# Kernel tuning notes

Hardware: AMD Instinct MI355X
Metric: run time of the kernel (lower is better)

## Reference

```python
import jax, jax.numpy as jnp
import numpy as np

N = 8192
F_IN = 512
F_HID = 256
ALPHA = 0.2  # LeakyReLU negative slope
NEG_INF = -9e15


def gat_layer(h, adj, W, a):
    """Standard dense GraphAttentionLayer (pyGAT style).
    h: [N, F_in], adj: [N, N] (0/1), W: [F_in, F_out], a: [2*F_out, 1].
    """
    Wh = h @ W  # [N, F_out]
    f_out = W.shape[1]
    # e_ij = leakyrelu(a1 . Wh_i + a2 . Wh_j) via broadcasting
    e1 = Wh @ a[:f_out]      # [N, 1]
    e2 = Wh @ a[f_out:]      # [N, 1]
    e = jax.nn.leaky_relu(e1 + e2.T, negative_slope=ALPHA)  # [N, N]
    e = jnp.where(adj > 0, e, NEG_INF)
    att = jax.nn.softmax(e, axis=-1)  # masked row softmax
    return jax.nn.elu(att @ Wh)       # [N, F_out]


def setup_inputs() -> dict:
    key = jax.random.key(0)
    k_x, k_adj, k_w1, k_a1, k_w2, k_a2 = jax.random.split(key, 6)
    x = jax.random.normal(k_x, (N, F_IN), dtype=jnp.float32)
    # sparse random adjacency (~avg degree 16) + self loops
    adj = (jax.random.uniform(k_adj, (N, N)) < (16.0 / N)).astype(jnp.float32)
    adj = jnp.clip(adj + jnp.eye(N, dtype=jnp.float32), 0.0, 1.0)
    # Xavier-ish init for layer params
    W1 = jax.random.normal(k_w1, (F_IN, F_HID), dtype=jnp.float32) * (1.0 / np.sqrt(F_IN))
    a1 = jax.random.normal(k_a1, (2 * F_HID, 1), dtype=jnp.float32) * (1.0 / np.sqrt(2 * F_HID))
    W2 = jax.random.normal(k_w2, (F_HID, F_IN), dtype=jnp.float32) * (1.0 / np.sqrt(F_HID))
    a2 = jax.random.normal(k_a2, (2 * F_IN, 1), dtype=jnp.float32) * (1.0 / np.sqrt(2 * F_IN))
    return {"x": x, "adj": adj, "W1": W1, "a1": a1, "W2": W2, "a2": a2}


def reference(x, adj, W1, a1, W2, a2):
    enc = gat_layer(x, adj, W1, a1)    # encode: [N, F_HID]
    dec = gat_layer(enc, adj, W2, a2)  # decode: [N, F_IN]
    return (dec, enc)
```

## Files before the change

kernel.cpp:

```cpp
#include <hip/hip_runtime.h>
#include <hip/hip_bf16.h>

#define N_NODES 8192
#define F_IN    512
#define F_HID   256
#define ALPHA   0.2f
#define MAXDEG  64

using f32x4 = __attribute__((ext_vector_type(4))) float;
using f16x8 = __attribute__((ext_vector_type(8))) _Float16;
using f16x4 = __attribute__((ext_vector_type(4))) _Float16;

__global__ void prep_kernel(const float* __restrict__ W1, const float* __restrict__ W2,
                            _Float16* __restrict__ W1T, _Float16* __restrict__ W2T,
                            const float* __restrict__ a2,
                            float* __restrict__ w2s, float* __restrict__ w2t,
                            float* __restrict__ stz) {
    const int tid = threadIdx.x;
    int gid = blockIdx.x * 256 + tid;
    if (gid < 2 * N_NODES) stz[gid] = 0.0f;

    if (blockIdx.x >= 256) {
        const int r = (blockIdx.x - 256) * 64 + (tid >> 2);
        const int q = tid & 3;
        float ss = 0.f, tt = 0.f;
        for (int n = q * 4; n < F_IN; n += 16) {
            f32x4 w  = *(const f32x4*)&W2[(size_t)r * F_IN + n];
            f32x4 as = *(const f32x4*)&a2[n];
            f32x4 at = *(const f32x4*)&a2[F_IN + n];
            #pragma unroll
            for (int j = 0; j < 4; ++j) { ss += w[j] * as[j]; tt += w[j] * at[j]; }
        }
        ss += __shfl_xor(ss, 1); ss += __shfl_xor(ss, 2);
        tt += __shfl_xor(tt, 1); tt += __shfl_xor(tt, 2);
        if (q == 0) { w2s[r] = ss; w2t[r] = tt; }
        return;
    }

    int t = blockIdx.x;
    const float* W; _Float16* WT; int K, N, kt, nt;
    if (t < 128) { W = W1; WT = W1T; K = 512; N = 256; kt = t & 15; nt = t >> 4; }
    else { t -= 128; W = W2; WT = W2T; K = 256; N = 512; kt = t & 7; nt = t >> 3; }
    __shared__ float Ws[32][33];
    const int tx = tid & 31, ty = tid >> 5;
    #pragma unroll
    for (int i = 0; i < 4; ++i)
        Ws[ty + 8 * i][tx] = W[(size_t)(kt * 32 + ty + 8 * i) * N + nt * 32 + tx];
    __syncthreads();
    #pragma unroll
    for (int i = 0; i < 4; ++i)
        WT[(size_t)(nt * 32 + ty + 8 * i) * K + kt * 32 + tx] = (_Float16)Ws[tx][ty + 8 * i];
}

__device__ inline void csr_row(const float* __restrict__ adj, int* __restrict__ cols,
                               int* __restrict__ cnt, int row, int lane) {
    const f32x4* arow = (const f32x4*)(adj + (size_t)row * N_NODES);
    int* crow = cols + (size_t)row * MAXDEG;
    int count = 0;
    const unsigned long long mlt = (1ULL << lane) - 1ULL;
    for (int base = 0; base < N_NODES; base += 512) {
        f32x4 v0 = __builtin_nontemporal_load(&arow[(base >> 2) + lane]);
        f32x4 v1 = __builtin_nontemporal_load(&arow[(base >> 2) + 64 + lane]);
        unsigned long long b0 = __ballot(v0[0] > 0.0f);
        unsigned long long b1 = __ballot(v0[1] > 0.0f);
        unsigned long long b2 = __ballot(v0[2] > 0.0f);
        unsigned long long b3 = __ballot(v0[3] > 0.0f);
        unsigned long long b4 = __ballot(v1[0] > 0.0f);
        unsigned long long b5 = __ballot(v1[1] > 0.0f);
        unsigned long long b6 = __ballot(v1[2] > 0.0f);
        unsigned long long b7 = __ballot(v1[3] > 0.0f);
        int o = count + __popcll(b0 & mlt) + __popcll(b1 & mlt)
                      + __popcll(b2 & mlt) + __popcll(b3 & mlt);
        int c0 = base + (lane << 2);
        if (v0[0] > 0.0f) { if (o < MAXDEG) crow[o] = c0;     o++; }
        if (v0[1] > 0.0f) { if (o < MAXDEG) crow[o] = c0 + 1; o++; }
        if (v0[2] > 0.0f) { if (o < MAXDEG) crow[o] = c0 + 2; o++; }
        if (v0[3] > 0.0f) { if (o < MAXDEG) crow[o] = c0 + 3; o++; }
        count += __popcll(b0) + __popcll(b1) + __popcll(b2) + __popcll(b3);
        o = count + __popcll(b4 & mlt) + __popcll(b5 & mlt)
                  + __popcll(b6 & mlt) + __popcll(b7 & mlt);
        int c1 = base + 256 + (lane << 2);
        if (v1[0] > 0.0f) { if (o < MAXDEG) crow[o] = c1;     o++; }
        if (v1[1] > 0.0f) { if (o < MAXDEG) crow[o] = c1 + 1; o++; }
        if (v1[2] > 0.0f) { if (o < MAXDEG) crow[o] = c1 + 2; o++; }
        if (v1[3] > 0.0f) { if (o < MAXDEG) crow[o] = c1 + 3; o++; }
        count += __popcll(b4) + __popcll(b5) + __popcll(b6) + __popcll(b7);
    }
    if (lane == 0) cnt[row] = count > MAXDEG ? MAXDEG : count;
}

__device__ inline void gemm1_tile(const float* __restrict__ x,
                                  const _Float16* __restrict__ W1T,
                                  _Float16* __restrict__ Wh1,
                                  const float* __restrict__ a1,
                                  float* __restrict__ s1, float* __restrict__ t1,
                                  int brow, int bcol) {
    const int LDT = 72;
    __shared__ _Float16 As[64 * LDT];
    __shared__ _Float16 Bs[128 * LDT];
    const int tid = threadIdx.x;
    const int wid = tid >> 6, lane = tid & 63;
    const int wr = (wid >> 1) * 32, wc = (wid & 1) * 64;
    const int sr = tid >> 3, skg = (tid & 7) * 8;

    f32x4 acc[2][4];
    #pragma unroll
    for (int m = 0; m < 2; ++m)
        #pragma unroll
        for (int n = 0; n < 4; ++n) acc[m][n] = f32x4{0.f, 0.f, 0.f, 0.f};

    for (int k0 = 0; k0 < F_IN; k0 += 64) {
        #pragma unroll
        for (int i = 0; i < 2; ++i) {
            int r = sr + i * 32;
            const f32x4* src = (const f32x4*)(x + (size_t)(brow + r) * F_IN + k0 + skg);
            f32x4 a0 = src[0];
            f32x4 a1v = src[1];
            f16x8 av;
            #pragma unroll
            for (int j = 0; j < 4; ++j) { av[j] = (_Float16)a0[j]; av[4 + j] = (_Float16)a1v[j]; }
            *(f16x8*)&As[r * LDT + skg] = av;
        }
        #pragma unroll
        for (int i = 0; i < 4; ++i) {
            int r = sr + i * 32;
            *(f16x8*)&Bs[r * LDT + skg] =
                *(const f16x8*)&W1T[(size_t)(bcol + r) * F_IN + k0 + skg];
        }
        __syncthreads();
        #pragma unroll
        for (int ks = 0; ks < 2; ++ks) {
            const int kb = ks * 32 + (lane >> 4) * 8;
            f16x8 af[2], bfr[4];
            #pragma unroll
            for (int m = 0; m < 2; ++m)
                af[m] = *(const f16x8*)&As[(wr + m * 16 + (lane & 15)) * LDT + kb];
            #pragma unroll
            for (int n = 0; n < 4; ++n)
                bfr[n] = *(const f16x8*)&Bs[(wc + n * 16 + (lane & 15)) * LDT + kb];
            #pragma unroll
            for (int m = 0; m < 2; ++m)
                #pragma unroll
                for (int n = 0; n < 4; ++n)
                    acc[m][n] = __builtin_amdgcn_mfma_f32_16x16x32_f16(
                        af[m], bfr[n], acc[m][n], 0, 0, 0);
        }
        __syncthreads();
    }
    const int cl = lane & 15;
    float as[4], at[4];
    #pragma unroll
    for (int n = 0; n < 4; ++n) {
        as[n] = a1[bcol + wc + n * 16 + cl];
        at[n] = a1[F_HID + bcol + wc + n * 16 + cl];
    }
    #pragma unroll
    for (int m = 0; m < 2; ++m) {
        #pragma unroll
        for (int j = 0; j < 4; ++j) {
            float vs = 0.f, vt = 0.f;
            #pragma unroll
            for (int n = 0; n < 4; ++n) { vs += acc[m][n][j] * as[n]; vt += acc[m][n][j] * at[n]; }
            #pragma unroll
            for (int off = 1; off < 16; off <<= 1) {
                vs += __shfl_xor(vs, off);
                vt += __shfl_xor(vt, off);
            }
            if (cl == 0) {
                int row = brow + wr + m * 16 + ((lane >> 4) << 2) + j;
                atomicAdd(s1 + row, vs);
                atomicAdd(t1 + row, vt);
            }
        }
        #pragma unroll
        for (int n = 0; n < 4; ++n) {
            int row = brow + wr + m * 16 + ((lane >> 4) << 2);
            int col = bcol + wc + n * 16 + cl;
            #pragma unroll
            for (int j = 0; j < 4; ++j)
                Wh1[(size_t)(row + j) * F_HID + col] = (_Float16)acc[m][n][j];
        }
    }
}

__global__ __launch_bounds__(256)
void csr_and_gemm1(const float* __restrict__ adj, int* __restrict__ cols,
                   int* __restrict__ cnt, const float* __restrict__ x,
                   const _Float16* __restrict__ W1T, _Float16* __restrict__ Wh1,
                   const float* __restrict__ a1,
                   float* __restrict__ s1, float* __restrict__ t1) {
    const int bid = blockIdx.x;
    if (bid < 256) {
        gemm1_tile(x, W1T, Wh1, a1, s1, t1, (bid & 127) * 64, (bid >> 7) * 128);
    } else {
        const int q = bid - 256;
        const int row = q * 4 + (threadIdx.x >> 6);
        csr_row(adj, cols, cnt, row, threadIdx.x & 63);
    }
}

__global__ void aggregate_l1(const _Float16* __restrict__ Wh,
                             const int* __restrict__ cols, const int* __restrict__ cnt,
                             const float* __restrict__ s, const float* __restrict__ t,
                             const float* __restrict__ w2s, const float* __restrict__ w2t,
                             float* __restrict__ enc, _Float16* __restrict__ enc16,
                             float* __restrict__ s2, float* __restrict__ t2) {
    const int wid = threadIdx.x >> 6, lane = threadIdx.x & 63;
    const int row = blockIdx.x * 4 + wid;
    const int deg = cnt[row];
    __shared__ float pS[4][64];
    __shared__ int jS[4][64];
    int j = 0;
    float ev = -1e30f;
    if (lane < deg) {
        j = cols[(size_t)row * MAXDEG + lane];
        float z = s[row] + t[j];
        ev = z > 0.0f ? z : ALPHA * z;
    }
    float m = ev;
    #pragma unroll
    for (int off = 32; off > 0; off >>= 1) m = fmaxf(m, __shfl_xor(m, off));
    float ex = (lane < deg) ? __expf(ev - m) : 0.0f;
    float sum = ex;
    #pragma unroll
    for (int off = 32; off > 0; off >>= 1) sum += __shfl_xor(sum, off);
    pS[wid][lane] = ex / sum;
    jS[wid][lane] = j;
    __syncthreads();

    float acc[4] = {};
    const size_t lo = (size_t)lane * 4;
    int d = 0;
    for (; d + 4 <= deg; d += 4) {
        float p0 = pS[wid][d],     p1 = pS[wid][d + 1];
        float p2 = pS[wid][d + 2], p3 = pS[wid][d + 3];
        f16x4 v0 = *(const f16x4*)(Wh + (size_t)jS[wid][d] * F_HID + lo);
        f16x4 v1 = *(const f16x4*)(Wh + (size_t)jS[wid][d + 1] * F_HID + lo);
        f16x4 v2 = *(const f16x4*)(Wh + (size_t)jS[wid][d + 2] * F_HID + lo);
        f16x4 v3 = *(const f16x4*)(Wh + (size_t)jS[wid][d + 3] * F_HID + lo);
        #pragma unroll
        for (int jj = 0; jj < 4; ++jj)
            acc[jj] += p0 * (float)v0[jj] + p1 * (float)v1[jj]
                     + p2 * (float)v2[jj] + p3 * (float)v3[jj];
    }
    for (; d < deg; ++d) {
        float p = pS[wid][d];
        f16x4 w = *(const f16x4*)(Wh + (size_t)jS[wid][d] * F_HID + lo);
        #pragma unroll
        for (int jj = 0; jj < 4; ++jj) acc[jj] += p * (float)w[jj];
    }
    f32x4 o; f16x4 h;
    #pragma unroll
    for (int jj = 0; jj < 4; ++jj) {
        float v = acc[jj];
        float e = v > 0.0f ? v : (__expf(v) - 1.0f);
        o[jj] = e; h[jj] = (_Float16)e;
    }
    __builtin_nontemporal_store(o, (f32x4*)(enc + (size_t)row * F_HID + lo));
    *(f16x4*)(enc16 + (size_t)row * F_HID + lo) = h;

    f32x4 ws = *(const f32x4*)(w2s + lo);
    f32x4 wt = *(const f32x4*)(w2t + lo);
    float ps = 0.f, pt = 0.f;
    #pragma unroll
    for (int jj = 0; jj < 4; ++jj) { ps += o[jj] * ws[jj]; pt += o[jj] * wt[jj]; }
    #pragma unroll
    for (int off = 32; off > 0; off >>= 1) {
        ps += __shfl_xor(ps, off);
        pt += __shfl_xor(pt, off);
    }
    if (lane == 0) { s2[row] = ps; t2[row] = pt; }
}

__global__ void aggregate_l2pre(const _Float16* __restrict__ enc16,
                                const int* __restrict__ cols, const int* __restrict__ cnt,
                                const float* __restrict__ s, const float* __restrict__ t,
                                _Float16* __restrict__ aggE16) {
    const int wid = threadIdx.x >> 6, lane = threadIdx.x & 63;
    const int row = blockIdx.x * 4 + wid;
    const int deg = cnt[row];
    __shared__ float pS[4][64];
    __shared__ int jS[4][64];
    int j = 0;
    float ev = -1e30f;
    if (lane < deg) {
        j = cols[(size_t)row * MAXDEG + lane];
        float z = s[row] + t[j];
        ev = z > 0.0f ? z : ALPHA * z;
    }
    float m = ev;
    #pragma unroll
    for (int off = 32; off > 0; off >>= 1) m = fmaxf(m, __shfl_xor(m, off));
    float ex = (lane < deg) ? __expf(ev - m) : 0.0f;
    float sum = ex;
    #pragma unroll
    for (int off = 32; off > 0; off >>= 1) sum += __shfl_xor(sum, off);
    pS[wid][lane] = ex / sum;
    jS[wid][lane] = j;
    __syncthreads();

    float acc[4] = {};
    const size_t lo = (size_t)lane * 4;
    int d = 0;
    for (; d + 4 <= deg; d += 4) {
        float p0 = pS[wid][d],     p1 = pS[wid][d + 1];
        float p2 = pS[wid][d + 2], p3 = pS[wid][d + 3];
        f16x4 v0 = *(const f16x4*)(enc16 + (size_t)jS[wid][d] * F_HID + lo);
        f16x4 v1 = *(const f16x4*)(enc16 + (size_t)jS[wid][d + 1] * F_HID + lo);
        f16x4 v2 = *(const f16x4*)(enc16 + (size_t)jS[wid][d + 2] * F_HID + lo);
        f16x4 v3 = *(const f16x4*)(enc16 + (size_t)jS[wid][d + 3] * F_HID + lo);
        #pragma unroll
        for (int jj = 0; jj < 4; ++jj)
            acc[jj] += p0 * (float)v0[jj] + p1 * (float)v1[jj]
                     + p2 * (float)v2[jj] + p3 * (float)v3[jj];
    }
    for (; d < deg; ++d) {
        float p = pS[wid][d];
        f16x4 w = *(const f16x4*)(enc16 + (size_t)jS[wid][d] * F_HID + lo);
        #pragma unroll
        for (int jj = 0; jj < 4; ++jj) acc[jj] += p * (float)w[jj];
    }
    f16x4 h;
    #pragma unroll
    for (int jj = 0; jj < 4; ++jj) h[jj] = (_Float16)acc[jj];
    *(f16x4*)(aggE16 + (size_t)row * F_HID + lo) = h;
}

__global__ __launch_bounds__(256)
void gemm2e(const _Float16* __restrict__ A, const _Float16* __restrict__ BT,
            float* __restrict__ C) {
    const int LDT = 72, LDB = 264;
    __shared__ _Float16 As[128 * LDT];
    __shared__ _Float16 Bs[64 * LDB];
    const int tid = threadIdx.x;
    const int wid = tid >> 6, lane = tid & 63;
    const int brow = (blockIdx.x >> 3) * 128;
    const int bcol = (blockIdx.x & 7) * 64;
    const int wr = (wid >> 1) * 64, wc = (wid & 1) * 32;

    #pragma unroll
    for (int i = 0; i < 8; ++i) {
        int id = tid + i * 256;
        int r = id >> 5, kc = (id & 31) * 8;
        *(f16x8*)&Bs[r * LDB + kc] = *(const f16x8*)&BT[(size_t)(bcol + r) * F_HID + kc];
    }

    f32x4 acc[4][2];
    #pragma unroll
    for (int m = 0; m < 4; ++m)
        #pragma unroll
        for (int n = 0; n < 2; ++n) acc[m][n] = f32x4{0.f, 0.f, 0.f, 0.f};

    for (int k0 = 0; k0 < F_HID; k0 += 64) {
        #pragma unroll
        for (int i = 0; i < 4; ++i) {
            int id = tid + i * 256;
            int r = id >> 3, kc = (id & 7) * 8;
            *(f16x8*)&As[r * LDT + kc] = *(const f16x8*)&A[(size_t)(brow + r) * F_HID + k0 + kc];
        }
        __syncthreads();
        #pragma unroll
        for (int ks = 0; ks < 2; ++ks) {
            const int kb = ks * 32 + (lane >> 4) * 8;
            f16x8 af[4], bfr[2];
            #pragma unroll
            for (int m = 0; m < 4; ++m)
                af[m] = *(const f16x8*)&As[(wr + m * 16 + (lane & 15)) * LDT + kb];
            #pragma unroll
            for (int n = 0; n < 2; ++n)
                bfr[n] = *(const f16x8*)&Bs[(wc + n * 16 + (lane & 15)) * LDB + k0 + kb];
            #pragma unroll
            for (int m = 0; m < 4; ++m)
                #pragma unroll
                for (int n = 0; n < 2; ++n)
                    acc[m][n] = __builtin_amdgcn_mfma_f32_16x16x32_f16(
                        af[m], bfr[n], acc[m][n], 0, 0, 0);
        }
        __syncthreads();
    }
    #pragma unroll
    for (int m = 0; m < 4; ++m)
        #pragma unroll
        for (int n = 0; n < 2; ++n) {
            int row = brow + wr + m * 16 + ((lane >> 4) << 2);
            int col = bcol + wc + n * 16 + (lane & 15);
            #pragma unroll
            for (int j = 0; j < 4; ++j) {
                float v = acc[m][n][j];
                float e = v > 0.0f ? v : (__expf(v) - 1.0f);
                __builtin_nontemporal_store(e, &C[(size_t)(row + j) * F_IN + col]);
            }
        }
}

extern "C" void kernel_launch(void* const* d_in, const int* in_sizes, int n_in,
                              void* d_out, int out_size, void* d_ws, size_t ws_size,
                              hipStream_t stream) {
    (void)in_sizes; (void)n_in; (void)out_size; (void)ws_size;
    const float* x   = (const float*)d_in[0];
    const float* adj = (const float*)d_in[1];
    const float* W1  = (const float*)d_in[2];
    const float* a1  = (const float*)d_in[3];
    const float* W2  = (const float*)d_in[4];
    const float* a2  = (const float*)d_in[5];

    float* dec = (float*)d_out;
    float* enc = dec + (size_t)N_NODES * F_IN;

    int*      cols   = (int*)d_ws;
    int*      cnt    = cols + (size_t)N_NODES * MAXDEG;
    float*    s1     = (float*)(cnt + N_NODES);
    float*    t1     = s1 + N_NODES;
    float*    s2     = t1 + N_NODES;
    float*    t2     = s2 + N_NODES;
    float*    w2s    = t2 + N_NODES;
    float*    w2t    = w2s + F_HID;
    _Float16* Wh1    = (_Float16*)(w2t + F_HID);
    _Float16* enc16  = Wh1 + (size_t)N_NODES * F_HID;
    _Float16* aggE16 = enc16 + (size_t)N_NODES * F_HID;
    _Float16* W1T    = aggE16 + (size_t)N_NODES * F_HID;
    _Float16* W2T    = W1T + (size_t)F_HID * F_IN;

    prep_kernel<<<260, 256, 0, stream>>>(W1, W2, W1T, W2T, a2, w2s, w2t, s1);

    csr_and_gemm1<<<2304, 256, 0, stream>>>(adj, cols, cnt, x, W1T, Wh1, a1, s1, t1);

    aggregate_l1<<<N_NODES / 4, 256, 0, stream>>>(Wh1, cols, cnt, s1, t1,
                                                  w2s, w2t, enc, enc16, s2, t2);

    aggregate_l2pre<<<N_NODES / 4, 256, 0, stream>>>(enc16, cols, cnt, s2, t2, aggE16);

    gemm2e<<<512, 256, 0, stream>>>(aggE16, W2T, dec);
}
```

Before: 100.3 us.

## Fold weight prep into front kernel and replace atomics with partial sums

Removes the separate prep kernel. W1 is now read as fp32 and transposed/converted into shared memory inside the GEMM1 tile, and the W2 transpose and the W2·a2 vectors are computed by extra blocks of the fused front kernel. The atomicAdd accumulation of s1/t1 becomes plain stores into four per-column-partition buffers, which aggregate_l1 sums, so the zero-init pass is no longer needed. This saves one launch and the atomic traffic. In exchange, the in-GEMM transpose does scalar strided shared-memory stores that may bank-conflict, and W1 conversion is repeated by every tile.

```diff
diff --git a/kernel.cpp b/kernel.cpp
--- a/kernel.cpp
+++ b/kernel.cpp
@@ -10,47 +10,6 @@
 using f32x4 = __attribute__((ext_vector_type(4))) float;
 using f16x8 = __attribute__((ext_vector_type(8))) _Float16;
 using f16x4 = __attribute__((ext_vector_type(4))) _Float16;
-
-__global__ void prep_kernel(const float* __restrict__ W1, const float* __restrict__ W2,
-                            _Float16* __restrict__ W1T, _Float16* __restrict__ W2T,
-                            const float* __restrict__ a2,
-                            float* __restrict__ w2s, float* __restrict__ w2t,
-                            float* __restrict__ stz) {
-    const int tid = threadIdx.x;
-    int gid = blockIdx.x * 256 + tid;
-    if (gid < 2 * N_NODES) stz[gid] = 0.0f;
-
-    if (blockIdx.x >= 256) {
-        const int r = (blockIdx.x - 256) * 64 + (tid >> 2);
-        const int q = tid & 3;
-        float ss = 0.f, tt = 0.f;
-        for (int n = q * 4; n < F_IN; n += 16) {
-            f32x4 w  = *(const f32x4*)&W2[(size_t)r * F_IN + n];
-            f32x4 as = *(const f32x4*)&a2[n];
-            f32x4 at = *(const f32x4*)&a2[F_IN + n];
-            #pragma unroll
-            for (int j = 0; j < 4; ++j) { ss += w[j] * as[j]; tt += w[j] * at[j]; }
-        }
-        ss += __shfl_xor(ss, 1); ss += __shfl_xor(ss, 2);
-        tt += __shfl_xor(tt, 1); tt += __shfl_xor(tt, 2);
-        if (q == 0) { w2s[r] = ss; w2t[r] = tt; }
-        return;
-    }
-
-    int t = blockIdx.x;
-    const float* W; _Float16* WT; int K, N, kt, nt;
-    if (t < 128) { W = W1; WT = W1T; K = 512; N = 256; kt = t & 15; nt = t >> 4; }
-    else { t -= 128; W = W2; WT = W2T; K = 256; N = 512; kt = t & 7; nt = t >> 3; }
-    __shared__ float Ws[32][33];
-    const int tx = tid & 31, ty = tid >> 5;
-    #pragma unroll
-    for (int i = 0; i < 4; ++i)
-        Ws[ty + 8 * i][tx] = W[(size_t)(kt * 32 + ty + 8 * i) * N + nt * 32 + tx];
-    __syncthreads();
-    #pragma unroll
-    for (int i = 0; i < 4; ++i)
-        WT[(size_t)(nt * 32 + ty + 8 * i) * K + kt * 32 + tx] = (_Float16)Ws[tx][ty + 8 * i];
-}
 
 __device__ inline void csr_row(const float* __restrict__ adj, int* __restrict__ cols,
                                int* __restrict__ cnt, int row, int lane) {
@@ -90,10 +49,10 @@
 }
 
 __device__ inline void gemm1_tile(const float* __restrict__ x,
-                                  const _Float16* __restrict__ W1T,
+                                  const float* __restrict__ W1,
                                   _Float16* __restrict__ Wh1,
                                   const float* __restrict__ a1,
-                                  float* __restrict__ s1, float* __restrict__ t1,
+                                  float* __restrict__ s1p, float* __restrict__ t1p,
                                   int brow, int bcol) {
     const int LDT = 72;
     __shared__ _Float16 As[64 * LDT];
@@ -121,11 +80,17 @@
             for (int j = 0; j < 4; ++j) { av[j] = (_Float16)a0[j]; av[4 + j] = (_Float16)a1v[j]; }
             *(f16x8*)&As[r * LDT + skg] = av;
         }
-        #pragma unroll
-        for (int i = 0; i < 4; ++i) {
-            int r = sr + i * 32;
-            *(f16x8*)&Bs[r * LDT + skg] =
-                *(const f16x8*)&W1T[(size_t)(bcol + r) * F_IN + k0 + skg];
+        {
+            const int cq = (tid & 31) * 4;
+            const int kbase = tid >> 5;
+            #pragma unroll
+            for (int rd = 0; rd < 8; ++rd) {
+                int krow = kbase + 8 * rd;
+                f32x4 w = *(const f32x4*)&W1[(size_t)(k0 + krow) * F_HID + bcol + cq];
+                #pragma unroll
+                for (int q = 0; q < 4; ++q)
+                    Bs[(cq + q) * LDT + krow] = (_Float16)w[q];
+            }
         }
         __syncthreads();
         #pragma unroll
@@ -148,6 +113,7 @@
         __syncthreads();
     }
     const int cl = lane & 15;
+    const int part = (bcol >> 7) * 2 + (wc >> 6);
     float as[4], at[4];
     #pragma unroll
     for (int n = 0; n < 4; ++n) {
@@ -168,8 +134,8 @@
             }
             if (cl == 0) {
                 int row = brow + wr + m * 16 + ((lane >> 4) << 2) + j;
-                atomicAdd(s1 + row, vs);
-                atomicAdd(t1 + row, vt);
+                s1p[part * N_NODES + row] = vs;
+                t1p[part * N_NODES + row] = vt;
             }
         }
         #pragma unroll
@@ -183,28 +149,144 @@
     }
 }
 
+__device__ inline void w2T_tile(int t, const float* __restrict__ W2,
+                                _Float16* __restrict__ W2T) {
+    __shared__ float Ws[32][33];
+    const int kt = t & 7, nt = t >> 3;
+    const int tx = threadIdx.x & 31, ty = threadIdx.x >> 5;
+    #pragma unroll
+    for (int i = 0; i < 4; ++i)
+        Ws[ty + 8 * i][tx] = W2[(size_t)(kt * 32 + ty + 8 * i) * F_IN + nt * 32 + tx];
+    __syncthreads();
+    #pragma unroll
+    for (int i = 0; i < 4; ++i)
+        W2T[(size_t)(nt * 32 + ty + 8 * i) * F_HID + kt * 32 + tx] = (_Float16)Ws[tx][ty + 8 * i];
+}
+
+__device__ inline void w2vec_job(int t, const float* __restrict__ W2,
+                                 const float* __restrict__ a2,
+                                 float* __restrict__ w2s, float* __restrict__ w2t) {
+    const int r = t * 64 + (threadIdx.x >> 2);
+    const int q = threadIdx.x & 3;
+    float ss = 0.f, tt = 0.f;
+    for (int n = q * 4; n < F_IN; n += 16) {
+        f32x4 w  = *(const f32x4*)&W2[(size_t)r * F_IN + n];
+        f32x4 as = *(const f32x4*)&a2[n];
+        f32x4 at = *(const f32x4*)&a2[F_IN + n];
+        #pragma unroll
+        for (int j = 0; j < 4; ++j) { ss += w[j] * as[j]; tt += w[j] * at[j]; }
+    }
+    ss += __shfl_xor(ss, 1); ss += __shfl_xor(ss, 2);
+    tt += __shfl_xor(tt, 1); tt += __shfl_xor(tt, 2);
+    if (q == 0) { w2s[r] = ss; w2t[r] = tt; }
+}
+
 __global__ __launch_bounds__(256)
-void csr_and_gemm1(const float* __restrict__ adj, int* __restrict__ cols,
-                   int* __restrict__ cnt, const float* __restrict__ x,
-                   const _Float16* __restrict__ W1T, _Float16* __restrict__ Wh1,
-                   const float* __restrict__ a1,
-                   float* __restrict__ s1, float* __restrict__ t1) {
+void front_kernel(const float* __restrict__ adj, int* __restrict__ cols,
+                  int* __restrict__ cnt, const float* __restrict__ x,
+                  const float* __restrict__ W1, const float* __restrict__ a1,
+                  _Float16* __restrict__ Wh1,
+                  float* __restrict__ s1p, float* __restrict__ t1p,
+                  const float* __restrict__ W2, const float* __restrict__ a2,
+                  _Float16* __restrict__ W2T,
+                  float* __restrict__ w2s, float* __restrict__ w2t) {
     const int bid = blockIdx.x;
     if (bid < 256) {
-        gemm1_tile(x, W1T, Wh1, a1, s1, t1, (bid & 127) * 64, (bid >> 7) * 128);
+        gemm1_tile(x, W1, Wh1, a1, s1p, t1p, (bid & 127) * 64, (bid >> 7) * 128);
+    } else if (bid < 384) {
+        w2T_tile(bid - 256, W2, W2T);
+    } else if (bid < 388) {
+        w2vec_job(bid - 384, W2, a2, w2s, w2t);
     } else {
-        const int q = bid - 256;
+        const int q = bid - 388;
         const int row = q * 4 + (threadIdx.x >> 6);
         csr_row(adj, cols, cnt, row, threadIdx.x & 63);
     }
 }
 
-__global__ void aggregate_l1(const _Float16* __restrict__ Wh,
-                             const int* __restrict__ cols, const int* __restrict__ cnt,
-                             const float* __restrict__ s, const float* __restrict__ t,
-                             const float* __restrict__ w2s, const float* __restrict__ w2t,
-                             float* __restrict__ enc, _Float16* __restrict__ enc16,
-                             float* __restrict__ s2, float* __restrict__ t2) {
+__global__ __launch_bounds__(256)
+void aggregate_l1(const _Float16* __restrict__ Wh,
+                  const int* __restrict__ cols, const int* __restrict__ cnt,
+                  const float* __restrict__ s1p, const float* __restrict__ t1p,
+                  const float* __restrict__ w2s, const float* __restrict__ w2t,
+                  float* __restrict__ enc, _Float16* __restrict__ enc16,
+                  float* __restrict__ s2, float* __restrict__ t2) {
+    const int wid = threadIdx.x >> 6, lane = threadIdx.x & 63;
+    const int row = blockIdx.x * 4 + wid;
+    const int deg = cnt[row];
+    __shared__ float pS[4][64];
+    __shared__ int jS[4][64];
+    const float sI = s1p[row] + s1p[N_NODES + row]
+                   + s1p[2 * N_NODES + row] + s1p[3 * N_NODES + row];
+    int j = 0;
+    float ev = -1e30f;
+    if (lane < deg) {
+        j = cols[(size_t)row * MAXDEG + lane];
+        float tj = t1p[j] + t1p[N_NODES + j]
+                 + t1p[2 * N_NODES + j] + t1p[3 * N_NODES + j];
+        float z = sI + tj;
+        ev = z > 0.0f ? z : ALPHA * z;
+    }
+    float m = ev;
+    #pragma unroll
+    for (int off = 32; off > 0; off >>= 1) m = fmaxf(m, __shfl_xor(m, off));
+    float ex = (lane < deg) ? __expf(ev - m) : 0.0f;
+    float sum = ex;
+    #pragma unroll
+    for (int off = 32; off > 0; off >>= 1) sum += __shfl_xor(sum, off);
+    pS[wid][lane] = ex / sum;
+    jS[wid][lane] = j;
+    __syncthreads();
+
+    float acc[4] = {};
+    const size_t lo = (size_t)lane * 4;
+    int d = 0;
+    for (; d + 4 <= deg; d += 4) {
+        float p0 = pS[wid][d],     p1 = pS[wid][d + 1];
+        float p2 = pS[wid][d + 2], p3 = pS[wid][d + 3];
+        f16x4 v0 = *(const f16x4*)(Wh + (size_t)jS[wid][d] * F_HID + lo);
+        f16x4 v1 = *(const f16x4*)(Wh + (size_t)jS[wid][d + 1] * F_HID + lo);
+        f16x4 v2 = *(const f16x4*)(Wh + (size_t)jS[wid][d + 2] * F_HID + lo);
+        f16x4 v3 = *(const f16x4*)(Wh + (size_t)jS[wid][d + 3] * F_HID + lo);
+        #pragma unroll
+        for (int jj = 0; jj < 4; ++jj)
+            acc[jj] += p0 * (float)v0[jj] + p1 * (float)v1[jj]
+                     + p2 * (float)v2[jj] + p3 * (float)v3[jj];
+    }
+    for (; d < deg; ++d) {
+        float p = pS[wid][d];
+        f16x4 w = *(const f16x4*)(Wh + (size_t)jS[wid][d] * F_HID + lo);
+        #pragma unroll
+        for (int jj = 0; jj < 4; ++jj) acc[jj] += p * (float)w[jj];
+    }
+    f32x4 o; f16x4 h;
+    #pragma unroll
+    for (int jj = 0; jj < 4; ++jj) {
+        float v = acc[jj];
+        float e = v > 0.0f ? v : (__expf(v) - 1.0f);
+        o[jj] = e; h[jj] = (_Float16)e;
+    }
+    __builtin_nontemporal_store(o, (f32x4*)(enc + (size_t)row * F_HID + lo));
+    *(f16x4*)(enc16 + (size_t)row * F_HID + lo) = h;
+
+    f32x4 ws = *(const f32x4*)(w2s + lo);
+    f32x4 wt = *(const f32x4*)(w2t + lo);
+    float ps = 0.f, pt = 0.f;
+    #pragma unroll
+    for (int jj = 0; jj < 4; ++jj) { ps += o[jj] * ws[jj]; pt += o[jj] * wt[jj]; }
+    #pragma unroll
+    for (int off = 32; off > 0; off >>= 1) {
+        ps += __shfl_xor(ps, off);
+        pt += __shfl_xor(pt, off);
+    }
+    if (lane == 0) { s2[row] = ps; t2[row] = pt; }
+}
+
+__global__ __launch_bounds__(256)
+void aggregate_l2pre(const _Float16* __restrict__ enc16,
+                     const int* __restrict__ cols, const int* __restrict__ cnt,
+                     const float* __restrict__ s, const float* __restrict__ t,
+                     _Float16* __restrict__ aggE16) {
     const int wid = threadIdx.x >> 6, lane = threadIdx.x & 63;
     const int row = blockIdx.x * 4 + wid;
     const int deg = cnt[row];
@@ -234,77 +316,6 @@
     for (; d + 4 <= deg; d += 4) {
         float p0 = pS[wid][d],     p1 = pS[wid][d + 1];
         float p2 = pS[wid][d + 2], p3 = pS[wid][d + 3];
-        f16x4 v0 = *(const f16x4*)(Wh + (size_t)jS[wid][d] * F_HID + lo);
-        f16x4 v1 = *(const f16x4*)(Wh + (size_t)jS[wid][d + 1] * F_HID + lo);
-        f16x4 v2 = *(const f16x4*)(Wh + (size_t)jS[wid][d + 2] * F_HID + lo);
-        f16x4 v3 = *(const f16x4*)(Wh + (size_t)jS[wid][d + 3] * F_HID + lo);
-        #pragma unroll
-        for (int jj = 0; jj < 4; ++jj)
-            acc[jj] += p0 * (float)v0[jj] + p1 * (float)v1[jj]
-                     + p2 * (float)v2[jj] + p3 * (float)v3[jj];
-    }
-    for (; d < deg; ++d) {
-        float p = pS[wid][d];
-        f16x4 w = *(const f16x4*)(Wh + (size_t)jS[wid][d] * F_HID + lo);
-        #pragma unroll
-        for (int jj = 0; jj < 4; ++jj) acc[jj] += p * (float)w[jj];
-    }
-    f32x4 o; f16x4 h;
-    #pragma unroll
-    for (int jj = 0; jj < 4; ++jj) {
-        float v = acc[jj];
-        float e = v > 0.0f ? v : (__expf(v) - 1.0f);
-        o[jj] = e; h[jj] = (_Float16)e;
-    }
-    __builtin_nontemporal_store(o, (f32x4*)(enc + (size_t)row * F_HID + lo));
-    *(f16x4*)(enc16 + (size_t)row * F_HID + lo) = h;
-
-    f32x4 ws = *(const f32x4*)(w2s + lo);
-    f32x4 wt = *(const f32x4*)(w2t + lo);
-    float ps = 0.f, pt = 0.f;
-    #pragma unroll
-    for (int jj = 0; jj < 4; ++jj) { ps += o[jj] * ws[jj]; pt += o[jj] * wt[jj]; }
-    #pragma unroll
-    for (int off = 32; off > 0; off >>= 1) {
-        ps += __shfl_xor(ps, off);
-        pt += __shfl_xor(pt, off);
-    }
-    if (lane == 0) { s2[row] = ps; t2[row] = pt; }
-}
-
-__global__ void aggregate_l2pre(const _Float16* __restrict__ enc16,
-                                const int* __restrict__ cols, const int* __restrict__ cnt,
-                                const float* __restrict__ s, const float* __restrict__ t,
-                                _Float16* __restrict__ aggE16) {
-    const int wid = threadIdx.x >> 6, lane = threadIdx.x & 63;
-    const int row = blockIdx.x * 4 + wid;
-    const int deg = cnt[row];
-    __shared__ float pS[4][64];
-    __shared__ int jS[4][64];
-    int j = 0;
-    float ev = -1e30f;
-    if (lane < deg) {
-        j = cols[(size_t)row * MAXDEG + lane];
-        float z = s[row] + t[j];
-        ev = z > 0.0f ? z : ALPHA * z;
-    }
-    float m = ev;
-    #pragma unroll
-    for (int off = 32; off > 0; off >>= 1) m = fmaxf(m, __shfl_xor(m, off));
-    float ex = (lane < deg) ? __expf(ev - m) : 0.0f;
-    float sum = ex;
-    #pragma unroll
-    for (int off = 32; off > 0; off >>= 1) sum += __shfl_xor(sum, off);
-    pS[wid][lane] = ex / sum;
-    jS[wid][lane] = j;
-    __syncthreads();
-
-    float acc[4] = {};
-    const size_t lo = (size_t)lane * 4;
-    int d = 0;
-    for (; d + 4 <= deg; d += 4) {
-        float p0 = pS[wid][d],     p1 = pS[wid][d + 1];
-        float p2 = pS[wid][d + 2], p3 = pS[wid][d + 3];
         f16x4 v0 = *(const f16x4*)(enc16 + (size_t)jS[wid][d] * F_HID + lo);
         f16x4 v1 = *(const f16x4*)(enc16 + (size_t)jS[wid][d + 1] * F_HID + lo);
         f16x4 v2 = *(const f16x4*)(enc16 + (size_t)jS[wid][d + 2] * F_HID + lo);
@@ -409,23 +420,21 @@
 
     int*      cols   = (int*)d_ws;
     int*      cnt    = cols + (size_t)N_NODES * MAXDEG;
-    float*    s1     = (float*)(cnt + N_NODES);
-    float*    t1     = s1 + N_NODES;
-    float*    s2     = t1 + N_NODES;
+    float*    s1p    = (float*)(cnt + N_NODES);
+    float*    t1p    = s1p + 4 * N_NODES;
+    float*    s2     = t1p + 4 * N_NODES;
     float*    t2     = s2 + N_NODES;
     float*    w2s    = t2 + N_NODES;
     float*    w2t    = w2s + F_HID;
     _Float16* Wh1    = (_Float16*)(w2t + F_HID);
     _Float16* enc16  = Wh1 + (size_t)N_NODES * F_HID;
     _Float16* aggE16 = enc16 + (size_t)N_NODES * F_HID;
-    _Float16* W1T    = aggE16 + (size_t)N_NODES * F_HID;
-    _Float16* W2T    = W1T + (size_t)F_HID * F_IN;
-
-    prep_kernel<<<260, 256, 0, stream>>>(W1, W2, W1T, W2T, a2, w2s, w2t, s1);
-
-    csr_and_gemm1<<<2304, 256, 0, stream>>>(adj, cols, cnt, x, W1T, Wh1, a1, s1, t1);
-
-    aggregate_l1<<<N_NODES / 4, 256, 0, stream>>>(Wh1, cols, cnt, s1, t1,
+    _Float16* W2T    = aggE16 + (size_t)N_NODES * F_HID;
+
+    front_kernel<<<2436, 256, 0, stream>>>(adj, cols, cnt, x, W1, a1, Wh1,
+                                           s1p, t1p, W2, a2, W2T, w2s, w2t);
+
+    aggregate_l1<<<N_NODES / 4, 256, 0, stream>>>(Wh1, cols, cnt, s1p, t1p,
                                                   w2s, w2t, enc, enc16, s2, t2);
 
     aggregate_l2pre<<<N_NODES / 4, 256, 0, stream>>>(enc16, cols, cnt, s2, t2, aggE16);
```

New measurement: 99.10 us (median of 2 runs). Within noise of the previous version (-1.2%).
